# Performance work log

Hardware: AMD Instinct MI355X
Metric: run time of the kernel (lower is better)

Reference implementation:

```python
import jax, jax.numpy as jnp
import numpy as np

D = 768
EXPAND = 4
D_INNER = EXPAND * D
G = 32
EPS = 1e-5


def setup_inputs() -> dict:
    key = jax.random.key(0)
    ks = jax.random.split(key, 10)
    B, T = 16, G * G
    s = lambda fan_in: 1.0 / np.sqrt(fan_in)
    return {
        "x": jax.random.normal(ks[0], (B, T, D), dtype=jnp.float32),
        "norm_w": jnp.ones((D,), dtype=jnp.float32),
        "w_proj": jax.random.normal(ks[1], (D_INNER, D), dtype=jnp.float32) * s(D),
        "w_gate": jax.random.normal(ks[2], (D_INNER, D), dtype=jnp.float32) * s(D),
        "conv_w": jax.random.normal(ks[3], (D_INNER, 1, 3, 3), dtype=jnp.float32) * s(9),
        "conv_b": jax.random.normal(ks[4], (D_INNER,), dtype=jnp.float32) * 0.01,
        "w_out": jax.random.normal(ks[5], (D, D_INNER), dtype=jnp.float32) * s(D_INNER),
        "w_k": jax.random.normal(ks[6], (D, D), dtype=jnp.float32) * s(D),
        "w_v": jax.random.normal(ks[7], (D, D), dtype=jnp.float32) * s(D),
        "log_alpha": jnp.array(0.0, dtype=jnp.float32),  # log(memory_alpha=1.0)
    }


def _rmsnorm(x, w):
    ms = jnp.mean(jnp.square(x.astype(jnp.float32)), axis=-1, keepdims=True)
    return x * jax.lax.rsqrt(ms + EPS).astype(x.dtype) * w


def reference(x, norm_w, w_proj, w_gate, conv_w, conv_b, w_out, w_k, w_v, log_alpha):
    B, T, _ = x.shape
    h = _rmsnorm(x, norm_w)                                   # [B,T,D]
    val = jnp.einsum("btd,ed->bte", h, w_proj)                # [B,T,dI]
    val = val.transpose(0, 2, 1).reshape(B, D_INNER, G, G)    # [B,dI,G,G]
    val = jax.lax.conv_general_dilated(
        val, conv_w, window_strides=(1, 1), padding=((1, 1), (1, 1)),
        dimension_numbers=("NCHW", "OIHW", "NCHW"),
        feature_group_count=D_INNER,
    ) + conv_b[None, :, None, None]
    val = jax.nn.silu(val)
    val = val.reshape(B, D_INNER, T).transpose(0, 2, 1)       # [B,T,dI]
    gated = val * jax.nn.silu(jnp.einsum("btd,ed->bte", h, w_gate))
    out = jnp.einsum("bte,de->btd", gated, w_out)             # [B,T,D]
    K = jnp.einsum("btd,ed->bte", h, w_k)                     # [B,T,D]
    V = jnp.einsum("btd,ed->bte", out, w_v)                   # [B,T,D]
    W = jnp.einsum("btd,bte->bde", K, V) / T                  # [B,D,D]
    read = jnp.einsum("btd,bde->bte", K, W)                   # [B,T,D]
    out = out + jnp.exp(log_alpha) * read
    return x + out
```

## Files before the change

kernel.cpp:

```cpp
#include <hip/hip_runtime.h>
#include <hip/hip_bf16.h>
#include <cstdint>
#include <cstddef>

typedef unsigned short u16;
typedef __attribute__((ext_vector_type(8))) __bf16 bf16x8;
typedef __attribute__((ext_vector_type(4))) float f32x4;

#define NDM 768
#define NDI 3072
#define NTT 1024
#define NBB 16
#define NM (NBB*NTT)

__device__ __forceinline__ u16 f2bf(float f) {
  unsigned u = __builtin_bit_cast(unsigned, f);
  u += 0x7fffu + ((u >> 16) & 1u);
  return (u16)(u >> 16);
}
__device__ __forceinline__ float bf2f(u16 b) {
  return __builtin_bit_cast(float, ((unsigned)b) << 16);
}
__device__ __forceinline__ float silu_f(float v) {
  return v * (1.0f / (1.0f + __expf(-v)));
}
__device__ __forceinline__ void gload16(const u16* g, u16* l) {
  __builtin_amdgcn_global_load_lds((const __attribute__((address_space(1))) void*)g,
                                   (__attribute__((address_space(3))) void*)l, 16, 0, 0);
}

__global__ __launch_bounds__(256)
void k_f32_to_bf16(const float* __restrict__ in, u16* __restrict__ out, int n4) {
  const int i = blockIdx.x * 256 + threadIdx.x;
  if (i < n4) {
    float4 v = ((const float4*)in)[i];
    ushort4 o;
    o.x = f2bf(v.x); o.y = f2bf(v.y); o.z = f2bf(v.z); o.w = f2bf(v.w);
    ((ushort4*)out)[i] = o;
  }
}

__global__ __launch_bounds__(256)
void k_convw_t(const float* __restrict__ cw, float* __restrict__ wT) {
  const int e = blockIdx.x * 256 + threadIdx.x;
  if (e < NDI) {
#pragma unroll
    for (int t = 0; t < 9; t++) wT[t * NDI + e] = cw[e * 9 + t];
  }
}

__global__ __launch_bounds__(256)
void k_rmsnorm(const float* __restrict__ x, const float* __restrict__ w, u16* __restrict__ h) {
  const int row  = blockIdx.x * 4 + (threadIdx.x >> 6);
  const int lane = threadIdx.x & 63;
  const float4* xr = (const float4*)(x + (size_t)row * NDM);
  float4 a = xr[lane], b = xr[lane + 64], c = xr[lane + 128];
  float ss = a.x*a.x + a.y*a.y + a.z*a.z + a.w*a.w
           + b.x*b.x + b.y*b.y + b.z*b.z + b.w*b.w
           + c.x*c.x + c.y*c.y + c.z*c.z + c.w*c.w;
#pragma unroll
  for (int off = 32; off > 0; off >>= 1) ss += __shfl_xor(ss, off);
  const float r = rsqrtf(ss * (1.0f / NDM) + 1e-5f);
  const float4* wr = (const float4*)w;
  float4 wa = wr[lane], wb = wr[lane + 64], wc = wr[lane + 128];
  ushort4 oa, ob, oc;
  oa.x = f2bf(a.x * r * wa.x); oa.y = f2bf(a.y * r * wa.y);
  oa.z = f2bf(a.z * r * wa.z); oa.w = f2bf(a.w * r * wa.w);
  ob.x = f2bf(b.x * r * wb.x); ob.y = f2bf(b.y * r * wb.y);
  ob.z = f2bf(b.z * r * wb.z); ob.w = f2bf(b.w * r * wb.w);
  oc.x = f2bf(c.x * r * wc.x); oc.y = f2bf(c.y * r * wc.y);
  oc.z = f2bf(c.z * r * wc.z); oc.w = f2bf(c.w * r * wc.w);
  ushort4* hr = (ushort4*)(h + (size_t)row * NDM);
  hr[lane] = oa; hr[lane + 64] = ob; hr[lane + 128] = oc;
}

template <int MODE>
__global__ __launch_bounds__(256)
void k_gemm_nt(const u16* __restrict__ A, const u16* __restrict__ B,
               void* __restrict__ C0, void* __restrict__ C1,
               const float* __restrict__ X, const float* __restrict__ scalep,
               int M, int N, int Kd,
               long sAb, long sBb, long sCb, int mPerBatchB, long sBm) {
  __shared__ u16 As[128 * 32];
  __shared__ u16 Bs[128 * 32];
  const int bz = blockIdx.z;
  A += (size_t)bz * sAb;
  B += (size_t)bz * sBb;
  const int m0 = blockIdx.y * 128, n0 = blockIdx.x * 128;
  if (mPerBatchB > 0) B += (size_t)(m0 / mPerBatchB) * sBm;

  const int lane = threadIdx.x & 63, wid = threadIdx.x >> 6;
  const int wm = wid >> 1, wn = wid & 1;

  f32x4 zero = {0.f, 0.f, 0.f, 0.f};
  f32x4 acc[4][4];
#pragma unroll
  for (int m = 0; m < 4; m++)
#pragma unroll
    for (int n = 0; n < 4; n++) acc[m][n] = zero;

  const u16* Ag = A + (size_t)(m0 + wid * 32 + (lane >> 2)) * Kd + (lane & 3) * 8;
  const u16* Bg = B + (size_t)(n0 + wid * 32 + (lane >> 2)) * Kd + (lane & 3) * 8;
  u16* AsW = &As[(wid * 32) * 32];
  u16* BsW = &Bs[(wid * 32) * 32];
  const int rowSkip = 16 * Kd;
  const int fr = lane & 15, fko = (lane >> 4) * 8;

  for (int kt = 0; kt < Kd; kt += 32) {
    gload16(Ag, AsW);
    gload16(Ag + rowSkip, AsW + 16 * 32);
    gload16(Bg, BsW);
    gload16(Bg + rowSkip, BsW + 16 * 32);
    Ag += 32; Bg += 32;
    __syncthreads();
    bf16x8 af[4], bfr[4];
#pragma unroll
    for (int m = 0; m < 4; m++)
      af[m] = *(const bf16x8*)&As[(wm * 64 + m * 16 + fr) * 32 + fko];
#pragma unroll
    for (int n = 0; n < 4; n++)
      bfr[n] = *(const bf16x8*)&Bs[(wn * 64 + n * 16 + fr) * 32 + fko];
#pragma unroll
    for (int m = 0; m < 4; m++)
#pragma unroll
      for (int n = 0; n < 4; n++)
        acc[m][n] = __builtin_amdgcn_mfma_f32_16x16x32_bf16(af[m], bfr[n], acc[m][n], 0, 0, 0);
    __syncthreads();
  }

  float sc = 1.0f;
  if (MODE == 2) sc = __expf(scalep[0]) * (1.0f / 1024.0f);
  const size_t cb = (size_t)bz * sCb;
#pragma unroll
  for (int m = 0; m < 4; m++) {
#pragma unroll
    for (int n = 0; n < 4; n++) {
      const int col = n0 + wn * 64 + n * 16 + (lane & 15);
      const int rb  = m0 + wm * 64 + m * 16 + ((lane >> 4) << 2);
#pragma unroll
      for (int q = 0; q < 4; q++) {
        const size_t idx = cb + (size_t)(rb + q) * N + col;
        const float v = acc[m][n][q];
        if (MODE == 0)      ((u16*)C0)[idx] = f2bf(v);
        else if (MODE == 1) { ((float*)C0)[idx] = v; ((u16*)C1)[idx] = f2bf(v); }
        else if (MODE == 2) ((u16*)C0)[idx] = f2bf(v * sc);
        else                ((float*)C0)[idx] = X[idx] + ((const float*)C1)[idx] + v;
      }
    }
  }
}

__global__ __launch_bounds__(384)
void k_conv_gate(const u16* __restrict__ val, u16* __restrict__ gate,
                 const float* __restrict__ wT, const float* __restrict__ bias) {
  const int m  = blockIdx.x;
  const int e0 = threadIdx.x * 8;
  const int j = m & 31, i = (m >> 5) & 31;
  float acc[8];
  {
    float4 b0 = *(const float4*)(bias + e0), b1 = *(const float4*)(bias + e0 + 4);
    acc[0] = b0.x; acc[1] = b0.y; acc[2] = b0.z; acc[3] = b0.w;
    acc[4] = b1.x; acc[5] = b1.y; acc[6] = b1.z; acc[7] = b1.w;
  }
  const u16* vb = val + (size_t)m * NDI + e0;
#pragma unroll
  for (int di = -1; di <= 1; di++) {
    const int ii = i + di;
    if (ii < 0 || ii >= 32) continue;
#pragma unroll
    for (int dj = -1; dj <= 1; dj++) {
      const int jj = j + dj;
      if (jj < 0 || jj >= 32) continue;
      const u16* vp = vb + (ptrdiff_t)(di * 32 + dj) * NDI;
      ushort4 v0 = *(const ushort4*)vp, v1 = *(const ushort4*)(vp + 4);
      const float* wp = wT + ((di + 1) * 3 + (dj + 1)) * NDI + e0;
      float4 w0 = *(const float4*)wp, w1 = *(const float4*)(wp + 4);
      acc[0] += bf2f(v0.x) * w0.x; acc[1] += bf2f(v0.y) * w0.y;
      acc[2] += bf2f(v0.z) * w0.z; acc[3] += bf2f(v0.w) * w0.w;
      acc[4] += bf2f(v1.x) * w1.x; acc[5] += bf2f(v1.y) * w1.y;
      acc[6] += bf2f(v1.z) * w1.z; acc[7] += bf2f(v1.w) * w1.w;
    }
  }
  u16* gp = gate + (size_t)m * NDI + e0;
  ushort4 g0 = *(const ushort4*)gp, g1 = *(const ushort4*)(gp + 4);
  ushort4 o0, o1;
  o0.x = f2bf(silu_f(acc[0]) * silu_f(bf2f(g0.x)));
  o0.y = f2bf(silu_f(acc[1]) * silu_f(bf2f(g0.y)));
  o0.z = f2bf(silu_f(acc[2]) * silu_f(bf2f(g0.z)));
  o0.w = f2bf(silu_f(acc[3]) * silu_f(bf2f(g0.w)));
  o1.x = f2bf(silu_f(acc[4]) * silu_f(bf2f(g1.x)));
  o1.y = f2bf(silu_f(acc[5]) * silu_f(bf2f(g1.y)));
  o1.z = f2bf(silu_f(acc[6]) * silu_f(bf2f(g1.z)));
  o1.w = f2bf(silu_f(acc[7]) * silu_f(bf2f(g1.w)));
  *(ushort4*)gp = o0;
  *(ushort4*)(gp + 4) = o1;
}

__global__ __launch_bounds__(256)
void k_transpose(const u16* __restrict__ in, u16* __restrict__ out) {
  __shared__ u16 tile[64][65];
  const int d0 = blockIdx.x * 64, t0 = blockIdx.y * 64, b = blockIdx.z;
  const int lx = threadIdx.x & 15, ly = threadIdx.x >> 4;
  const u16* ip = in + ((size_t)b * NTT + t0) * NDM + d0;
#pragma unroll
  for (int p = 0; p < 4; p++) {
    const int r = ly + p * 16;
    ushort4 v = *(const ushort4*)(ip + (size_t)r * NDM + lx * 4);
    tile[r][lx * 4 + 0] = v.x; tile[r][lx * 4 + 1] = v.y;
    tile[r][lx * 4 + 2] = v.z; tile[r][lx * 4 + 3] = v.w;
  }
  __syncthreads();
  u16* op = out + ((size_t)b * NDM + d0) * NTT + t0;
#pragma unroll
  for (int p = 0; p < 4; p++) {
    const int r = ly + p * 16;
    ushort4 v;
    v.x = tile[lx * 4 + 0][r]; v.y = tile[lx * 4 + 1][r];
    v.z = tile[lx * 4 + 2][r]; v.w = tile[lx * 4 + 3][r];
    *(ushort4*)(op + (size_t)r * NTT + lx * 4) = v;
  }
}

extern "C" void kernel_launch(void* const* d_in, const int* in_sizes, int n_in,
                              void* d_out, int out_size, void* d_ws, size_t ws_size,
                              hipStream_t stream) {
  const float* x      = (const float*)d_in[0];
  const float* norm_w = (const float*)d_in[1];
  const float* w_proj = (const float*)d_in[2];
  const float* w_gate = (const float*)d_in[3];
  const float* conv_w = (const float*)d_in[4];
  const float* conv_b = (const float*)d_in[5];
  const float* w_out  = (const float*)d_in[6];
  const float* w_k    = (const float*)d_in[7];
  const float* w_v    = (const float*)d_in[8];
  const float* lalpha = (const float*)d_in[9];

  char* ob = (char*)d_out;
  u16*   h   = (u16*)(ob);
  u16*   wpb = (u16*)(ob + 25165824);
  u16*   wgb = (u16*)(ob + 29884416);
  u16*   wob = (u16*)(ob + 34603008);
  u16*   wkb = (u16*)(ob + 39321600);
  u16*   wvb = (u16*)(ob + 40501248);
  float* wT  = (float*)(ob + 41680896);

  char* ws = (char*)d_ws;
  u16*   valp  = (u16*)(ws);
  u16*   gateb = (u16*)(ws + 100663296);
  float* outf  = (float*)(ws);
  u16*   outb  = (u16*)(ws + 50331648);
  u16*   Kbf   = (u16*)(ws + 75497472);
  u16*   Vbf   = (u16*)(ws + 100663296);
  u16*   Kt    = (u16*)(ws + 125829120);
  u16*   Vt    = (u16*)(ws + 150994944);
  u16*   Wt    = (u16*)(ws + 176160768);

  k_f32_to_bf16<<<2304, 256, 0, stream>>>(w_proj, wpb, 589824);
  k_f32_to_bf16<<<2304, 256, 0, stream>>>(w_gate, wgb, 589824);
  k_f32_to_bf16<<<2304, 256, 0, stream>>>(w_out,  wob, 589824);
  k_f32_to_bf16<<<576,  256, 0, stream>>>(w_k,    wkb, 147456);
  k_f32_to_bf16<<<576,  256, 0, stream>>>(w_v,    wvb, 147456);
  k_convw_t<<<12, 256, 0, stream>>>(conv_w, wT);

  k_rmsnorm<<<4096, 256, 0, stream>>>(x, norm_w, h);

  k_gemm_nt<0><<<dim3(24, 128, 1), 256, 0, stream>>>(h, wpb, valp, nullptr, nullptr, nullptr,
                                                     NM, NDI, NDM, 0, 0, 0, 0, 0);
  k_gemm_nt<0><<<dim3(24, 128, 1), 256, 0, stream>>>(h, wgb, gateb, nullptr, nullptr, nullptr,
                                                     NM, NDI, NDM, 0, 0, 0, 0, 0);
  k_conv_gate<<<NM, 384, 0, stream>>>(valp, gateb, wT, conv_b);

  k_gemm_nt<1><<<dim3(6, 128, 1), 256, 0, stream>>>(gateb, wob, outf, outb, nullptr, nullptr,
                                                    NM, NDM, NDI, 0, 0, 0, 0, 0);
  k_gemm_nt<0><<<dim3(6, 128, 1), 256, 0, stream>>>(h, wkb, Kbf, nullptr, nullptr, nullptr,
                                                    NM, NDM, NDM, 0, 0, 0, 0, 0);
  k_gemm_nt<0><<<dim3(6, 128, 1), 256, 0, stream>>>(outb, wvb, Vbf, nullptr, nullptr, nullptr,
                                                    NM, NDM, NDM, 0, 0, 0, 0, 0);
  k_transpose<<<dim3(12, 16, 16), 256, 0, stream>>>(Kbf, Kt);
  k_transpose<<<dim3(12, 16, 16), 256, 0, stream>>>(Vbf, Vt);

  k_gemm_nt<2><<<dim3(6, 6, 16), 256, 0, stream>>>(Vt, Kt, Wt, nullptr, nullptr, lalpha,
                                                   NDM, NDM, NTT,
                                                   (long)NDM * NTT, (long)NDM * NTT,
                                                   (long)NDM * NDM, 0, 0);
  k_gemm_nt<3><<<dim3(6, 128, 1), 256, 0, stream>>>(Kbf, Wt, d_out, outf, x, nullptr,
                                                    NM, NDM, NDM, 0, 0, 0,
                                                    NTT, (long)NDM * NDM);
}
```

Measured before the change: 815.3 us.

## Fuse proj/gate GEMMs, add swizzled 1D tile mapping, widen conv-gate kernel

Concatenates w_proj and w_gate into one weight so a single GEMM produces both val and the silu-applied gate. The silu on the gate moves into the GEMM epilogue. The out GEMM now writes only bf16, and the final residual reads that bf16 copy instead of an fp32 one, which lowers output precision slightly. GEMMs switch to a 1D grid with an XCD-style block swizzle meant to improve L2 locality. The conv-gate kernel now uses bf16 conv weights and processes 16 channels per thread with two rows per block, cutting memory traffic and launch count.

```diff
diff --git a/kernel.cpp b/kernel.cpp
--- a/kernel.cpp
+++ b/kernel.cpp
@@ -6,6 +6,7 @@
 typedef unsigned short u16;
 typedef __attribute__((ext_vector_type(8))) __bf16 bf16x8;
 typedef __attribute__((ext_vector_type(4))) float f32x4;
+typedef __attribute__((ext_vector_type(8))) unsigned short us8;
 
 #define NDM 768
 #define NDI 3072
@@ -41,11 +42,11 @@
 }
 
 __global__ __launch_bounds__(256)
-void k_convw_t(const float* __restrict__ cw, float* __restrict__ wT) {
+void k_convw_t(const float* __restrict__ cw, u16* __restrict__ wTb) {
   const int e = blockIdx.x * 256 + threadIdx.x;
   if (e < NDI) {
 #pragma unroll
-    for (int t = 0; t < 9; t++) wT[t * NDI + e] = cw[e * 9 + t];
+    for (int t = 0; t < 9; t++) wTb[t * NDI + e] = f2bf(cw[e * 9 + t]);
   }
 }
 
@@ -79,14 +80,19 @@
 void k_gemm_nt(const u16* __restrict__ A, const u16* __restrict__ B,
                void* __restrict__ C0, void* __restrict__ C1,
                const float* __restrict__ X, const float* __restrict__ scalep,
-               int M, int N, int Kd,
+               int N, int Kd, int nTiles,
                long sAb, long sBb, long sCb, int mPerBatchB, long sBm) {
   __shared__ u16 As[128 * 32];
   __shared__ u16 Bs[128 * 32];
   const int bz = blockIdx.z;
   A += (size_t)bz * sAb;
   B += (size_t)bz * sBb;
-  const int m0 = blockIdx.y * 128, n0 = blockIdx.x * 128;
+
+  const int nwg = gridDim.x;
+  const int id = blockIdx.x;
+  const int sid = ((nwg & 7) == 0) ? ((id & 7) * (nwg >> 3) + (id >> 3)) : id;
+  const int mt = sid / nTiles, nt = sid - mt * nTiles;
+  const int m0 = mt * 128, n0 = nt * 128;
   if (mPerBatchB > 0) B += (size_t)(m0 / mPerBatchB) * sBm;
 
   const int lane = threadIdx.x & 63, wid = threadIdx.x >> 6;
@@ -139,12 +145,18 @@
       const int rb  = m0 + wm * 64 + m * 16 + ((lane >> 4) << 2);
 #pragma unroll
       for (int q = 0; q < 4; q++) {
-        const size_t idx = cb + (size_t)(rb + q) * N + col;
         const float v = acc[m][n][q];
-        if (MODE == 0)      ((u16*)C0)[idx] = f2bf(v);
-        else if (MODE == 1) { ((float*)C0)[idx] = v; ((u16*)C1)[idx] = f2bf(v); }
-        else if (MODE == 2) ((u16*)C0)[idx] = f2bf(v * sc);
-        else                ((float*)C0)[idx] = X[idx] + ((const float*)C1)[idx] + v;
+        if (MODE == 0) {
+          ((u16*)C0)[cb + (size_t)(rb + q) * N + col] = f2bf(v);
+        } else if (MODE == 2) {
+          ((u16*)C0)[cb + (size_t)(rb + q) * N + col] = f2bf(v * sc);
+        } else if (MODE == 3) {
+          const size_t idx = (size_t)(rb + q) * N + col;
+          ((float*)C0)[idx] = X[idx] + bf2f(((const u16*)C1)[idx]) + v;
+        } else {
+          if (n0 < 3072) ((u16*)C0)[(size_t)(rb + q) * 3072 + col] = f2bf(v);
+          else           ((u16*)C1)[(size_t)(rb + q) * 3072 + (col - 3072)] = f2bf(silu_f(v));
+        }
       }
     }
   }
@@ -152,48 +164,46 @@
 
 __global__ __launch_bounds__(384)
 void k_conv_gate(const u16* __restrict__ val, u16* __restrict__ gate,
-                 const float* __restrict__ wT, const float* __restrict__ bias) {
-  const int m  = blockIdx.x;
-  const int e0 = threadIdx.x * 8;
+                 const u16* __restrict__ wTb, const float* __restrict__ bias) {
+  const int tid = threadIdx.x;
+  const int m = blockIdx.x * 2 + (tid >= 192);
+  const int e0 = (tid % 192) * 16;
   const int j = m & 31, i = (m >> 5) & 31;
-  float acc[8];
+  float acc[16];
   {
-    float4 b0 = *(const float4*)(bias + e0), b1 = *(const float4*)(bias + e0 + 4);
-    acc[0] = b0.x; acc[1] = b0.y; acc[2] = b0.z; acc[3] = b0.w;
-    acc[4] = b1.x; acc[5] = b1.y; acc[6] = b1.z; acc[7] = b1.w;
+    const float4* bp = (const float4*)(bias + e0);
+    float4 b0 = bp[0], b1 = bp[1], b2 = bp[2], b3 = bp[3];
+    acc[0]=b0.x; acc[1]=b0.y; acc[2]=b0.z; acc[3]=b0.w;
+    acc[4]=b1.x; acc[5]=b1.y; acc[6]=b1.z; acc[7]=b1.w;
+    acc[8]=b2.x; acc[9]=b2.y; acc[10]=b2.z; acc[11]=b2.w;
+    acc[12]=b3.x; acc[13]=b3.y; acc[14]=b3.z; acc[15]=b3.w;
   }
   const u16* vb = val + (size_t)m * NDI + e0;
 #pragma unroll
   for (int di = -1; di <= 1; di++) {
-    const int ii = i + di;
-    if (ii < 0 || ii >= 32) continue;
+    if ((unsigned)(i + di) >= 32u) continue;
 #pragma unroll
     for (int dj = -1; dj <= 1; dj++) {
-      const int jj = j + dj;
-      if (jj < 0 || jj >= 32) continue;
+      if ((unsigned)(j + dj) >= 32u) continue;
       const u16* vp = vb + (ptrdiff_t)(di * 32 + dj) * NDI;
-      ushort4 v0 = *(const ushort4*)vp, v1 = *(const ushort4*)(vp + 4);
-      const float* wp = wT + ((di + 1) * 3 + (dj + 1)) * NDI + e0;
-      float4 w0 = *(const float4*)wp, w1 = *(const float4*)(wp + 4);
-      acc[0] += bf2f(v0.x) * w0.x; acc[1] += bf2f(v0.y) * w0.y;
-      acc[2] += bf2f(v0.z) * w0.z; acc[3] += bf2f(v0.w) * w0.w;
-      acc[4] += bf2f(v1.x) * w1.x; acc[5] += bf2f(v1.y) * w1.y;
-      acc[6] += bf2f(v1.z) * w1.z; acc[7] += bf2f(v1.w) * w1.w;
+      us8 v0 = *(const us8*)vp, v1 = *(const us8*)(vp + 8);
+      const u16* wp = wTb + ((di + 1) * 3 + (dj + 1)) * NDI + e0;
+      us8 w0 = *(const us8*)wp, w1 = *(const us8*)(wp + 8);
+#pragma unroll
+      for (int q = 0; q < 8; q++) acc[q]     += bf2f(v0[q]) * bf2f(w0[q]);
+#pragma unroll
+      for (int q = 0; q < 8; q++) acc[8 + q] += bf2f(v1[q]) * bf2f(w1[q]);
     }
   }
   u16* gp = gate + (size_t)m * NDI + e0;
-  ushort4 g0 = *(const ushort4*)gp, g1 = *(const ushort4*)(gp + 4);
-  ushort4 o0, o1;
-  o0.x = f2bf(silu_f(acc[0]) * silu_f(bf2f(g0.x)));
-  o0.y = f2bf(silu_f(acc[1]) * silu_f(bf2f(g0.y)));
-  o0.z = f2bf(silu_f(acc[2]) * silu_f(bf2f(g0.z)));
-  o0.w = f2bf(silu_f(acc[3]) * silu_f(bf2f(g0.w)));
-  o1.x = f2bf(silu_f(acc[4]) * silu_f(bf2f(g1.x)));
-  o1.y = f2bf(silu_f(acc[5]) * silu_f(bf2f(g1.y)));
-  o1.z = f2bf(silu_f(acc[6]) * silu_f(bf2f(g1.z)));
-  o1.w = f2bf(silu_f(acc[7]) * silu_f(bf2f(g1.w)));
-  *(ushort4*)gp = o0;
-  *(ushort4*)(gp + 4) = o1;
+  us8 g0 = *(const us8*)gp, g1 = *(const us8*)(gp + 8);
+  us8 o0, o1;
+#pragma unroll
+  for (int q = 0; q < 8; q++) o0[q] = f2bf(silu_f(acc[q]) * bf2f(g0[q]));
+#pragma unroll
+  for (int q = 0; q < 8; q++) o1[q] = f2bf(silu_f(acc[8 + q]) * bf2f(g1[q]));
+  *(us8*)gp = o0;
+  *(us8*)(gp + 8) = o1;
 }
 
 __global__ __launch_bounds__(256)
@@ -236,54 +246,50 @@
   const float* lalpha = (const float*)d_in[9];
 
   char* ob = (char*)d_out;
-  u16*   h   = (u16*)(ob);
-  u16*   wpb = (u16*)(ob + 25165824);
-  u16*   wgb = (u16*)(ob + 29884416);
-  u16*   wob = (u16*)(ob + 34603008);
-  u16*   wkb = (u16*)(ob + 39321600);
-  u16*   wvb = (u16*)(ob + 40501248);
-  float* wT  = (float*)(ob + 41680896);
+  u16* h    = (u16*)(ob);
+  u16* wcat = (u16*)(ob + 25165824);
+  u16* wob  = (u16*)(ob + 34603008);
+  u16* wkb  = (u16*)(ob + 39321600);
+  u16* wvb  = (u16*)(ob + 40501248);
+  u16* wTb  = (u16*)(ob + 41680896);
 
   char* ws = (char*)d_ws;
-  u16*   valp  = (u16*)(ws);
-  u16*   gateb = (u16*)(ws + 100663296);
-  float* outf  = (float*)(ws);
-  u16*   outb  = (u16*)(ws + 50331648);
-  u16*   Kbf   = (u16*)(ws + 75497472);
-  u16*   Vbf   = (u16*)(ws + 100663296);
-  u16*   Kt    = (u16*)(ws + 125829120);
-  u16*   Vt    = (u16*)(ws + 150994944);
-  u16*   Wt    = (u16*)(ws + 176160768);
-
-  k_f32_to_bf16<<<2304, 256, 0, stream>>>(w_proj, wpb, 589824);
-  k_f32_to_bf16<<<2304, 256, 0, stream>>>(w_gate, wgb, 589824);
+  u16* valp  = (u16*)(ws);
+  u16* gateb = (u16*)(ws + 100663296);
+  u16* outb  = (u16*)(ws);
+  u16* Kbf   = (u16*)(ws + 25165824);
+  u16* Vbf   = (u16*)(ws + 50331648);
+  u16* Kt    = (u16*)(ws + 100663296);
+  u16* Vt    = (u16*)(ws + 125829120);
+  u16* Wt    = (u16*)(ws + 150994944);
+
+  k_f32_to_bf16<<<2304, 256, 0, stream>>>(w_proj, wcat,           589824);
+  k_f32_to_bf16<<<2304, 256, 0, stream>>>(w_gate, wcat + 2359296, 589824);
   k_f32_to_bf16<<<2304, 256, 0, stream>>>(w_out,  wob, 589824);
   k_f32_to_bf16<<<576,  256, 0, stream>>>(w_k,    wkb, 147456);
   k_f32_to_bf16<<<576,  256, 0, stream>>>(w_v,    wvb, 147456);
-  k_convw_t<<<12, 256, 0, stream>>>(conv_w, wT);
+  k_convw_t<<<12, 256, 0, stream>>>(conv_w, wTb);
 
   k_rmsnorm<<<4096, 256, 0, stream>>>(x, norm_w, h);
 
-  k_gemm_nt<0><<<dim3(24, 128, 1), 256, 0, stream>>>(h, wpb, valp, nullptr, nullptr, nullptr,
-                                                     NM, NDI, NDM, 0, 0, 0, 0, 0);
-  k_gemm_nt<0><<<dim3(24, 128, 1), 256, 0, stream>>>(h, wgb, gateb, nullptr, nullptr, nullptr,
-                                                     NM, NDI, NDM, 0, 0, 0, 0, 0);
-  k_conv_gate<<<NM, 384, 0, stream>>>(valp, gateb, wT, conv_b);
-
-  k_gemm_nt<1><<<dim3(6, 128, 1), 256, 0, stream>>>(gateb, wob, outf, outb, nullptr, nullptr,
-                                                    NM, NDM, NDI, 0, 0, 0, 0, 0);
-  k_gemm_nt<0><<<dim3(6, 128, 1), 256, 0, stream>>>(h, wkb, Kbf, nullptr, nullptr, nullptr,
-                                                    NM, NDM, NDM, 0, 0, 0, 0, 0);
-  k_gemm_nt<0><<<dim3(6, 128, 1), 256, 0, stream>>>(outb, wvb, Vbf, nullptr, nullptr, nullptr,
-                                                    NM, NDM, NDM, 0, 0, 0, 0, 0);
+  k_gemm_nt<5><<<6144, 256, 0, stream>>>(h, wcat, valp, gateb, nullptr, nullptr,
+                                         6144, NDM, 48, 0, 0, 0, 0, 0);
+  k_conv_gate<<<8192, 384, 0, stream>>>(valp, gateb, wTb, conv_b);
+
+  k_gemm_nt<0><<<768, 256, 0, stream>>>(gateb, wob, outb, nullptr, nullptr, nullptr,
+                                        NDM, NDI, 6, 0, 0, 0, 0, 0);
+  k_gemm_nt<0><<<768, 256, 0, stream>>>(h, wkb, Kbf, nullptr, nullptr, nullptr,
+                                        NDM, NDM, 6, 0, 0, 0, 0, 0);
+  k_gemm_nt<0><<<768, 256, 0, stream>>>(outb, wvb, Vbf, nullptr, nullptr, nullptr,
+                                        NDM, NDM, 6, 0, 0, 0, 0, 0);
   k_transpose<<<dim3(12, 16, 16), 256, 0, stream>>>(Kbf, Kt);
   k_transpose<<<dim3(12, 16, 16), 256, 0, stream>>>(Vbf, Vt);
 
-  k_gemm_nt<2><<<dim3(6, 6, 16), 256, 0, stream>>>(Vt, Kt, Wt, nullptr, nullptr, lalpha,
-                                                   NDM, NDM, NTT,
-                                                   (long)NDM * NTT, (long)NDM * NTT,
-                                                   (long)NDM * NDM, 0, 0);
-  k_gemm_nt<3><<<dim3(6, 128, 1), 256, 0, stream>>>(Kbf, Wt, d_out, outf, x, nullptr,
-                                                    NM, NDM, NDM, 0, 0, 0,
-                                                    NTT, (long)NDM * NDM);
-}
+  k_gemm_nt<2><<<dim3(36, 1, 16), 256, 0, stream>>>(Vt, Kt, Wt, nullptr, nullptr, lalpha,
+                                                    NDM, NTT, 6,
+                                                    (long)NDM * NTT, (long)NDM * NTT,
+                                                    (long)NDM * NDM, 0, 0);
+  k_gemm_nt<3><<<768, 256, 0, stream>>>(Kbf, Wt, d_out, outb, x, nullptr,
+                                        NDM, NDM, 6, 0, 0, 0,
+                                        NTT, (long)NDM * NDM);
+}
```

Measured after the change: 749.5 us. -8.1%, faster.
